# Kernel tuning notes

Measured on AMD Instinct MI355X. Metric: run time of the kernel, lower is better.

The kernel has to match this reference:

```python
import math
import jax, jax.numpy as jnp
import numpy as np

B, T, C, H = 2, 2048, 1024, 16
HD = C // H
ALPHA = 32.0


def setup_inputs() -> dict:
    key = jax.random.key(0)
    ks = jax.random.split(key, 16)
    s = 0.02
    inp = {
        "query": jax.random.normal(ks[0], (B, T, C), jnp.float32),
        "key": jax.random.normal(ks[1], (B, T, C), jnp.float32),
        "value": jax.random.normal(ks[2], (B, T, C), jnp.float32),
        # causal mask: 0 => masked (matches masked_fill(att_mask == 0, -inf))
        "att_mask": jnp.tril(jnp.ones((1, 1, T, T), jnp.float32)),
        "Wq": jax.random.normal(ks[3], (C, C), jnp.float32) * s,
        "bq": jnp.zeros((C,), jnp.float32),
        "Wk": jax.random.normal(ks[4], (C, C), jnp.float32) * s,
        "bk": jnp.zeros((C,), jnp.float32),
        "Wv": jax.random.normal(ks[5], (C, C), jnp.float32) * s,
        "bv": jnp.zeros((C,), jnp.float32),
        "Wp": jax.random.normal(ks[6], (C, C), jnp.float32) * s,
        "bp": jnp.zeros((C,), jnp.float32),
    }
    return inp


def reference(query, key, value, att_mask, Wq, bq, Wk, bk, Wv, bv, Wp, bp):
    b, tq, c = query.shape
    tk = key.shape[1]
    # separate QKV projections, split heads: [B,H,T,HD]
    q = (query @ Wq + bq).reshape(b, tq, H, HD).transpose(0, 2, 1, 3)
    k = (key @ Wk + bk).reshape(b, tk, H, HD).transpose(0, 2, 1, 3)
    v = (value @ Wv + bv).reshape(b, tk, H, HD).transpose(0, 2, 1, 3)
    # PBrelax: pre-scale q by 1/(alpha*sqrt(hd)), subtract detached global abs-max, rescale
    att = jnp.einsum("bhqd,bhkd->bhqk", q * (1.0 / ALPHA / math.sqrt(HD)), k)
    att = (att - jax.lax.stop_gradient(jnp.max(jnp.abs(att)))) * ALPHA
    att = jnp.where(att_mask[:, :, :tq, :tk] == 0, -jnp.inf, att)
    att = jax.nn.softmax(att, axis=-1)
    y = jnp.einsum("bhqk,bhkd->bhqd", att, v)
    y = y.transpose(0, 2, 1, 3).reshape(b, tq, c)
    return y @ Wp + bp
```

## Files before the change

kernel.cpp:

```cpp
#include <hip/hip_runtime.h>


#define Bsz 2
#define Tsz 2048
#define Csz 1024
#define Hsz 16
#define HDsz 64

typedef __bf16 bf16;
typedef __bf16 bf16x8 __attribute__((ext_vector_type(8)));
typedef __bf16 bf16x4 __attribute__((ext_vector_type(4)));
typedef float float4v __attribute__((ext_vector_type(4)));

#define MFMA16(a, b, c) __builtin_amdgcn_mfma_f32_16x16x32_bf16(a, b, c, 0, 0, 0)

#define GLOAD_LDS16(gptr, lptr)                                      \
  __builtin_amdgcn_global_load_lds(                                  \
      (const __attribute__((address_space(1))) void*)(gptr),         \
      (__attribute__((address_space(3))) void*)(lptr), 16, 0, 0)

__global__ __launch_bounds__(256) void cast3_bf16(
    const float* __restrict__ q, const float* __restrict__ k,
    const float* __restrict__ v, bf16* __restrict__ oq,
    bf16* __restrict__ ok, bf16* __restrict__ ov) {
  const int z = blockIdx.z;
  const float* src = z == 0 ? q : (z == 1 ? k : v);
  bf16* dst = z == 0 ? oq : (z == 1 ? ok : ov);
  const size_t i = ((size_t)blockIdx.x * 256 + threadIdx.x) * 8;
  const float4 a = *(const float4*)(src + i);
  const float4 b = *(const float4*)(src + i + 4);
  bf16x8 o;
  o[0] = (bf16)a.x; o[1] = (bf16)a.y; o[2] = (bf16)a.z; o[3] = (bf16)a.w;
  o[4] = (bf16)b.x; o[5] = (bf16)b.y; o[6] = (bf16)b.z; o[7] = (bf16)b.w;
  *(bf16x8*)(dst + i) = o;
}

__global__ __launch_bounds__(256) void wtrans_bf16(
    const float* __restrict__ Wq, const float* __restrict__ Wk,
    const float* __restrict__ Wv, const float* __restrict__ Wp,
    bf16* __restrict__ WT) {
  const int z = blockIdx.z;
  const float* W = z == 0 ? Wq : (z == 1 ? Wk : (z == 2 ? Wv : Wp));
  bf16* out = WT + (size_t)z * (Csz * Csz);
  __shared__ float Ts[64][68];
  const int k0 = blockIdx.y * 64, n0 = blockIdx.x * 64;
  const int tid = threadIdx.x;
#pragma unroll
  for (int it = 0; it < 4; ++it) {
    const int idx = it * 256 + tid;
    const int r = idx >> 4, c4 = (idx & 15) * 4;
    *(float4*)&Ts[r][c4] = *(const float4*)(W + (size_t)(k0 + r) * Csz + n0 + c4);
  }
  __syncthreads();
#pragma unroll
  for (int it = 0; it < 2; ++it) {
    const int idx = it * 256 + tid;
    const int n = idx & 63, k8 = (idx >> 6) * 8;
    bf16x8 o;
#pragma unroll
    for (int j = 0; j < 8; ++j) o[j] = (bf16)Ts[k8 + j][n];
    *(bf16x8*)(out + (size_t)(n0 + n) * Csz + k0 + k8) = o;
  }
}

__global__ __launch_bounds__(512, 2) void gemm256_qkv(
    const bf16* __restrict__ A0, const bf16* __restrict__ A1,
    const bf16* __restrict__ A2, const bf16* __restrict__ Wt,
    const float* __restrict__ b0, const float* __restrict__ b1,
    const float* __restrict__ b2, bf16* __restrict__ C0,
    bf16* __restrict__ C1, bf16* __restrict__ Vt) {
  constexpr int NT = Csz / 64;
  const int z = blockIdx.z;
  const bf16* A = z == 0 ? A0 : (z == 1 ? A1 : A2);
  const float* bias = z == 0 ? b0 : (z == 1 ? b1 : b2);
  const bf16* Bt = Wt + (size_t)z * (Csz * Csz);
  const int m0 = blockIdx.y * 256;
  const int nz0 = blockIdx.x * 256;

  __shared__ bf16 As[2 * 256 * 64];
  __shared__ bf16 Bs[2 * 256 * 64];

  const int tid = threadIdx.x;
  const int wave = tid >> 6, lane = tid & 63;
  const int l15 = lane & 15, quad = lane >> 4;
  const int wm = wave >> 2, wn = wave & 3;

  const int srow = tid >> 3;
  const int sch = tid & 7;
  const bf16* Ab = A + (size_t)(m0 + srow) * Csz + (sch ^ (srow & 7)) * 8;
  const bf16* Bb = Bt + (size_t)(nz0 + srow) * Csz + (sch ^ (srow & 7)) * 8;

#define STG(Xb, lds, lbuf, hh, tt)                                           \
  {                                                                          \
    GLOAD_LDS16((Xb) + (size_t)((hh)*128) * Csz + (size_t)(tt)*64,           \
                &(lds)[(lbuf) * (256 * 64) + (hh)*8192 + tid * 8]);          \
    GLOAD_LDS16((Xb) + (size_t)((hh)*128 + 64) * Csz + (size_t)(tt)*64,     \
                &(lds)[(lbuf) * (256 * 64) + (hh)*8192 + 4096 + tid * 8]);  \
  }
#define RD_A(dst, lbuf, i2, ks)                                              \
  dst = *(const bf16x8*)&As[(lbuf) * (256 * 64) +                            \
                            (wm * 128 + (i2)*16 + l15) * 64 +                \
                            ((((ks)*4 + quad) ^ (l15 & 7)) * 8)];
#define RD_B(dst, lbuf, j2, ks)                                              \
  dst = *(const bf16x8*)&Bs[(lbuf) * (256 * 64) +                            \
                            (wn * 64 + (j2)*16 + l15) * 64 +                 \
                            ((((ks)*4 + quad) ^ (l15 & 7)) * 8)];

  float4v acc[8][4];
#pragma unroll
  for (int i = 0; i < 8; ++i)
#pragma unroll
    for (int j = 0; j < 4; ++j) acc[i][j] = (float4v){0.f, 0.f, 0.f, 0.f};

  STG(Ab, As, 0, 0, 0);
  STG(Ab, As, 0, 1, 0);
  STG(Bb, Bs, 0, 0, 0);
  STG(Bb, Bs, 0, 1, 0);
  STG(Ab, As, 1, 0, 1);
  STG(Ab, As, 1, 1, 1);
  asm volatile("s_waitcnt vmcnt(4)" ::: "memory");
  __builtin_amdgcn_s_barrier();
  __builtin_amdgcn_sched_barrier(0);

#pragma unroll 1
  for (int t = 0; t < NT; ++t) {
    const int bsel = t & 1;
    bf16x8 af0[4][2], af1[4][2], bf0[2][2], bf1[2][2];

#pragma unroll
    for (int i = 0; i < 4; ++i) {
      RD_A(af0[i][0], bsel, i, 0);
      RD_A(af0[i][1], bsel, i, 1);
    }
#pragma unroll
    for (int j = 0; j < 2; ++j) {
      RD_B(bf0[j][0], bsel, j, 0);
      RD_B(bf0[j][1], bsel, j, 1);
    }
    if (t + 1 < NT) STG(Bb, Bs, bsel ^ 1, 0, t + 1);
    __builtin_amdgcn_s_barrier();
    asm volatile("s_waitcnt lgkmcnt(0)" ::: "memory");
    __builtin_amdgcn_sched_barrier(0);
    __builtin_amdgcn_s_setprio(1);
#pragma unroll
    for (int i = 0; i < 4; ++i)
#pragma unroll
      for (int j = 0; j < 2; ++j) {
        acc[i][j] = MFMA16(af0[i][0], bf0[j][0], acc[i][j]);
        acc[i][j] = MFMA16(af0[i][1], bf0[j][1], acc[i][j]);
      }
    __builtin_amdgcn_s_setprio(0);
    __builtin_amdgcn_s_barrier();

#pragma unroll
    for (int i = 0; i < 4; ++i) {
      RD_A(af1[i][0], bsel, 4 + i, 0);
      RD_A(af1[i][1], bsel, 4 + i, 1);
    }
    if (t + 1 < NT) STG(Bb, Bs, bsel ^ 1, 1, t + 1);
    __builtin_amdgcn_s_barrier();
    asm volatile("s_waitcnt lgkmcnt(0)" ::: "memory");
    __builtin_amdgcn_sched_barrier(0);
    __builtin_amdgcn_s_setprio(1);
#pragma unroll
    for (int i = 0; i < 4; ++i)
#pragma unroll
      for (int j = 0; j < 2; ++j) {
        acc[4 + i][j] = MFMA16(af1[i][0], bf0[j][0], acc[4 + i][j]);
        acc[4 + i][j] = MFMA16(af1[i][1], bf0[j][1], acc[4 + i][j]);
      }
    __builtin_amdgcn_s_setprio(0);
    __builtin_amdgcn_s_barrier();

#pragma unroll
    for (int j = 0; j < 2; ++j) {
      RD_B(bf1[j][0], bsel, 2 + j, 0);
      RD_B(bf1[j][1], bsel, 2 + j, 1);
    }
    if (t + 2 < NT) STG(Ab, As, bsel, 0, t + 2);
    __builtin_amdgcn_s_barrier();
    asm volatile("s_waitcnt lgkmcnt(0)" ::: "memory");
    __builtin_amdgcn_sched_barrier(0);
    __builtin_amdgcn_s_setprio(1);
#pragma unroll
    for (int i = 0; i < 4; ++i)
#pragma unroll
      for (int j = 0; j < 2; ++j) {
        acc[i][2 + j] = MFMA16(af0[i][0], bf1[j][0], acc[i][2 + j]);
        acc[i][2 + j] = MFMA16(af0[i][1], bf1[j][1], acc[i][2 + j]);
      }
    __builtin_amdgcn_s_setprio(0);
    __builtin_amdgcn_s_barrier();

    if (t + 2 < NT) STG(Ab, As, bsel, 1, t + 2);
    __builtin_amdgcn_s_barrier();
    __builtin_amdgcn_s_setprio(1);
#pragma unroll
    for (int i = 0; i < 4; ++i)
#pragma unroll
      for (int j = 0; j < 2; ++j) {
        acc[4 + i][2 + j] = MFMA16(af1[i][0], bf1[j][0], acc[4 + i][2 + j]);
        acc[4 + i][2 + j] = MFMA16(af1[i][1], bf1[j][1], acc[4 + i][2 + j]);
      }
    __builtin_amdgcn_s_setprio(0);
    if (t + 2 < NT) {
      asm volatile("s_waitcnt vmcnt(4)" ::: "memory");
    } else if (t + 1 < NT) {
      asm volatile("s_waitcnt vmcnt(0)" ::: "memory");
    }
    __builtin_amdgcn_s_barrier();
    __builtin_amdgcn_sched_barrier(0);
  }
#undef STG
#undef RD_A
#undef RD_B

  const int omb0 = m0 + wm * 128 + quad * 4;
  const int onb0 = nz0 + wn * 64 + l15;
  if (z == 2) {
#pragma unroll
    for (int j = 0; j < 4; ++j) {
      const int n = onb0 + j * 16;
      const float bj = bias[n];
#pragma unroll
      for (int i = 0; i < 8; ++i) {
        const int mrow = omb0 + i * 16;
        const int bb = mrow >> 11, tt = mrow & (Tsz - 1);
        union { bf16 h[4]; uint2 u; } pk;
#pragma unroll
        for (int r = 0; r < 4; ++r) pk.h[r] = (bf16)(acc[i][j][r] + bj);
        *(uint2*)(Vt + ((size_t)(bb * 1024 + n)) * Tsz + tt) = pk.u;
      }
    }
  } else {
    bf16* C = z == 0 ? C0 : C1;
    const float osc = z == 0 ? 0.180336880111124f : 1.0f;
#pragma unroll
    for (int j = 0; j < 4; ++j) {
      const float bj = bias[onb0 + j * 16];
#pragma unroll
      for (int i = 0; i < 8; ++i) {
#pragma unroll
        for (int r = 0; r < 4; ++r) {
          const float v = (acc[i][j][r] + bj) * osc;
          C[(size_t)(omb0 + i * 16 + r) * Csz + onb0 + j * 16] = (bf16)v;
        }
      }
    }
  }
}

template <typename OutT, bool VTR>
__global__ __launch_bounds__(256) void gemm_mfma(
    const bf16* __restrict__ A0, const bf16* __restrict__ A1,
    const bf16* __restrict__ A2, const bf16* __restrict__ Wt,
    const float* __restrict__ b0, const float* __restrict__ b1,
    const float* __restrict__ b2, OutT* __restrict__ C0,
    OutT* __restrict__ C1, OutT* __restrict__ C2, int M, int N, int K) {
  const int z = blockIdx.z;
  const bf16* A = z == 0 ? A0 : (z == 1 ? A1 : A2);
  const float* bias = z == 0 ? b0 : (z == 1 ? b1 : b2);
  OutT* C = z == 0 ? C0 : (z == 1 ? C1 : C2);
  const bf16* Bt = Wt + (size_t)z * N * K;
  const float osc = (VTR && z == 0) ? 0.180336880111124f : 1.0f;

  __shared__ bf16 As[128 * 32];
  __shared__ bf16 Bs[128 * 32];
  const int tid = threadIdx.x;
  const int wave = tid >> 6, lane = tid & 63;
  const int l15 = lane & 15, quad = lane >> 4;
  const int m0 = blockIdx.y * 128, n0 = blockIdx.x * 128;
  const int wm = (wave >> 1) * 64, wn = (wave & 1) * 64;
  const int srow = tid >> 2, schunk = tid & 3;

  float4v acc[4][4];
#pragma unroll
  for (int i = 0; i < 4; ++i)
#pragma unroll
    for (int j = 0; j < 4; ++j) acc[i][j] = (float4v){0.f, 0.f, 0.f, 0.f};

  for (int k0 = 0; k0 < K; k0 += 32) {
    __syncthreads();
#pragma unroll
    for (int p = 0; p < 2; ++p) {
      const int row = p * 64 + srow;
      GLOAD_LDS16(A + (size_t)(m0 + row) * K + k0 + schunk * 8,
                  &As[(p * 256 + tid) * 8]);
      GLOAD_LDS16(Bt + (size_t)(n0 + row) * K + k0 + schunk * 8,
                  &Bs[(p * 256 + tid) * 8]);
    }
    __syncthreads();

    bf16x8 af[4], bfr[4];
#pragma unroll
    for (int i = 0; i < 4; ++i)
      af[i] = *(const bf16x8*)&As[(wm + i * 16 + l15) * 32 + quad * 8];
#pragma unroll
    for (int j = 0; j < 4; ++j)
      bfr[j] = *(const bf16x8*)&Bs[(wn + j * 16 + l15) * 32 + quad * 8];
#pragma unroll
    for (int i = 0; i < 4; ++i)
#pragma unroll
      for (int j = 0; j < 4; ++j)
        acc[i][j] = MFMA16(af[i], bfr[j], acc[i][j]);
  }

  const int omb = m0 + wm + quad * 4;
  const int onb = n0 + wn + l15;
  if (VTR && z == 2) {
#pragma unroll
    for (int j = 0; j < 4; ++j) {
      const int n = onb + j * 16;
      const float bj = bias[n];
#pragma unroll
      for (int i = 0; i < 4; ++i) {
        const int mrow = omb + i * 16;
        const int bb = mrow >> 11, t = mrow & (Tsz - 1);
        union { bf16 h[4]; uint2 u; } pk;
#pragma unroll
        for (int r = 0; r < 4; ++r) pk.h[r] = (bf16)(acc[i][j][r] + bj);
        *(uint2*)((bf16*)C + ((size_t)(bb * 1024 + n)) * Tsz + t) = pk.u;
      }
    }
  } else {
#pragma unroll
    for (int j = 0; j < 4; ++j) {
      const float bj = bias[onb + j * 16];
#pragma unroll
      for (int i = 0; i < 4; ++i) {
#pragma unroll
        for (int r = 0; r < 4; ++r) {
          const float v = (acc[i][j][r] + bj) * osc;
          const size_t off = (size_t)(omb + i * 16 + r) * N + onb + j * 16;
          if constexpr (sizeof(OutT) == 2)
            C[off] = (OutT)v;
          else
            C[off] = v;
        }
      }
    }
  }
}

__global__ __launch_bounds__(256) void attn_mfma(const bf16* __restrict__ Q,
                                                 const bf16* __restrict__ K,
                                                 const bf16* __restrict__ Vt,
                                                 bf16* __restrict__ Y) {
  __shared__ bf16 Ks[2][64 * 64];
  __shared__ bf16 Vs[2][64 * 64];
  __shared__ bf16 Ps[4][32 * 72];

  const int bh = blockIdx.y;
  const int b = bh >> 4, h = bh & 15;
  const int i0 = (int)(gridDim.x - 1 - blockIdx.x) * 128;
  const int tid = threadIdx.x;
  const int wave = tid >> 6, lane = tid & 63;
  const int l15 = lane & 15, quad = lane >> 4;

  const int srow = tid >> 3;
  const int sch = tid & 7;

  const bf16* kb = K + (size_t)b * Tsz * Csz + h * HDsz;
  const bf16* vb = Vt + (size_t)bh * HDsz * Tsz;

  const int qb = i0 + wave * 32;

  bf16x8 qf[2][2];
#pragma unroll
  for (int sub = 0; sub < 2; ++sub) {
    const bf16* qp =
        Q + ((size_t)(b * Tsz + qb + sub * 16 + l15)) * Csz + h * HDsz + quad * 8;
    qf[sub][0] = *(const bf16x8*)qp;
    qf[sub][1] = *(const bf16x8*)(qp + 32);
  }

  bf16x8 ones;
#pragma unroll
  for (int j = 0; j < 8; ++j) ones[j] = (bf16)1.0f;

  float4v Of[2][4];
  float4v accl[2];
#pragma unroll
  for (int sub = 0; sub < 2; ++sub) {
    accl[sub] = (float4v){0.f, 0.f, 0.f, 0.f};
#pragma unroll
    for (int nc = 0; nc < 4; ++nc) Of[sub][nc] = (float4v){0.f, 0.f, 0.f, 0.f};
  }

  const int ntile = i0 / 64 + 2;

#pragma unroll
  for (int p = 0; p < 2; ++p) {
    const int r = p * 32 + srow;
    const int c = sch ^ (r & 7);
    GLOAD_LDS16(kb + (size_t)r * Csz + c * 8, &Ks[0][(p * 256 + tid) * 8]);
    GLOAD_LDS16(vb + (size_t)r * Tsz + c * 8, &Vs[0][(p * 256 + tid) * 8]);
  }

  for (int t = 0; t < ntile; ++t) {
    const int j0 = t * 64;
    const int buf = t & 1;
    __syncthreads();
    if (t + 1 < ntile) {
#pragma unroll
      for (int p = 0; p < 2; ++p) {
        const int r = p * 32 + srow;
        const int c = sch ^ (r & 7);
        GLOAD_LDS16(kb + (size_t)(j0 + 64 + r) * Csz + c * 8,
                    &Ks[buf ^ 1][(p * 256 + tid) * 8]);
        GLOAD_LDS16(vb + (size_t)r * Tsz + (j0 + 64) + c * 8,
                    &Vs[buf ^ 1][(p * 256 + tid) * 8]);
      }
    }

    if (j0 <= qb + 31) {
      float4v S[2][4];
#pragma unroll
      for (int nc = 0; nc < 4; ++nc) {
        const int row = nc * 16 + l15;
        const bf16x8 k0 =
            *(const bf16x8*)&Ks[buf][row * 64 + ((quad ^ (row & 7)) * 8)];
        const bf16x8 k1 =
            *(const bf16x8*)&Ks[buf][row * 64 + (((quad + 4) ^ (row & 7)) * 8)];
#pragma unroll
        for (int sub = 0; sub < 2; ++sub) {
          float4v a = (float4v){0.f, 0.f, 0.f, 0.f};
          a = MFMA16(k0, qf[sub][0], a);
          a = MFMA16(k1, qf[sub][1], a);
          S[sub][nc] = a;
        }
      }

      if (j0 + 63 > qb) {
#pragma unroll
        for (int sub = 0; sub < 2; ++sub) {
          const int q = qb + sub * 16 + l15;
#pragma unroll
          for (int nc = 0; nc < 4; ++nc) {
            const int keyb = j0 + nc * 16 + quad * 4;
#pragma unroll
            for (int r = 0; r < 4; ++r)
              if (keyb + r > q) S[sub][nc][r] = -1e30f;
          }
        }
      }

#pragma unroll
      for (int sub = 0; sub < 2; ++sub) {
#pragma unroll
        for (int nc = 0; nc < 4; ++nc) {
          bf16x4 pk;
#pragma unroll
          for (int r = 0; r < 4; ++r)
            pk[r] = (bf16)__builtin_amdgcn_exp2f(S[sub][nc][r]);
          *(bf16x4*)&Ps[wave][(sub * 16 + l15) * 72 + nc * 16 + quad * 4] = pk;
        }
      }

      bf16x8 pf[2][2];
#pragma unroll
      for (int sub = 0; sub < 2; ++sub) {
#pragma unroll
        for (int kc = 0; kc < 2; ++kc)
          pf[sub][kc] = *(const bf16x8*)
              &Ps[wave][(sub * 16 + l15) * 72 + kc * 32 + quad * 8];
        accl[sub] = MFMA16(ones, pf[sub][0], accl[sub]);
        accl[sub] = MFMA16(ones, pf[sub][1], accl[sub]);
      }
#pragma unroll
      for (int nc = 0; nc < 4; ++nc) {
        const int row = nc * 16 + l15;
#pragma unroll
        for (int kc = 0; kc < 2; ++kc) {
          const bf16x8 vf = *(const bf16x8*)
              &Vs[buf][row * 64 + (((kc * 4 + quad) ^ (row & 7)) * 8)];
#pragma unroll
          for (int sub = 0; sub < 2; ++sub)
            Of[sub][nc] = MFMA16(vf, pf[sub][kc], Of[sub][nc]);
        }
      }
    }
  }

#pragma unroll
  for (int sub = 0; sub < 2; ++sub) {
    const float rl = __builtin_amdgcn_rcpf(accl[sub][0]);
    const size_t rowoff =
        ((size_t)(b * Tsz + qb + sub * 16 + l15)) * Csz + h * HDsz;
#pragma unroll
    for (int nc = 0; nc < 4; ++nc) {
      union { bf16 h4[4]; uint2 u; } pk;
#pragma unroll
      for (int r = 0; r < 4; ++r) pk.h4[r] = (bf16)(Of[sub][nc][r] * rl);
      *(uint2*)(Y + rowoff + nc * 16 + quad * 4) = pk.u;
    }
  }
}

extern "C" void kernel_launch(void* const* d_in, const int* in_sizes, int n_in,
                              void* d_out, int out_size, void* d_ws,
                              size_t ws_size, hipStream_t stream) {
  const float* query = (const float*)d_in[0];
  const float* key = (const float*)d_in[1];
  const float* value = (const float*)d_in[2];
  const float* Wq = (const float*)d_in[4];
  const float* bq = (const float*)d_in[5];
  const float* Wk = (const float*)d_in[6];
  const float* bk = (const float*)d_in[7];
  const float* Wv = (const float*)d_in[8];
  const float* bv = (const float*)d_in[9];
  const float* Wp = (const float*)d_in[10];
  const float* bp = (const float*)d_in[11];
  float* out = (float*)d_out;

  char* ws = (char*)d_ws;
  bf16* WT = (bf16*)(ws);
  bf16* vc = (bf16*)(ws + (8u << 20));
  bf16* Qp = (bf16*)(ws + (16u << 20));
  bf16* Kp = (bf16*)(ws + (24u << 20));
  bf16* Vt = (bf16*)(ws + (32u << 20));
  bf16* Yb = vc;
  bf16* qc = (bf16*)d_out;
  bf16* kc = (bf16*)((char*)d_out + (8u << 20));

  const int M = Bsz * Tsz;

  cast3_bf16<<<dim3((M * Csz) / (256 * 8), 1, 3), dim3(256), 0, stream>>>(
      query, key, value, qc, kc, vc);
  wtrans_bf16<<<dim3(16, 16, 4), dim3(256), 0, stream>>>(Wq, Wk, Wv, Wp, WT);
  gemm256_qkv<<<dim3(Csz / 256, M / 256, 3), dim3(512), 0, stream>>>(
      qc, kc, vc, WT, bq, bk, bv, Qp, Kp, Vt);
  attn_mfma<<<dim3(Tsz / 128, Bsz * Hsz), dim3(256), 0, stream>>>(Qp, Kp, Vt,
                                                                  Yb);
  gemm_mfma<float, false><<<dim3(Csz / 128, M / 128, 1), dim3(256), 0, stream>>>(
      Yb, Yb, Yb, WT + 3u * (Csz * Csz), bp, bp, bp, out, out, out, M, Csz,
      Csz);
}
```

Baseline: 257.0 us.

## Triple-buffer K/V tiles with explicit vmcnt waits and balance causal block order

Moves the attention kernel's K/V staging from double to triple buffering and prefetches two tiles ahead. Partial vmcnt waits plus raw s_barrier replace __syncthreads, so the next tile's loads can stay in flight while the current tile is computed. It also interleaves query-block indices (long and short causal rows alternate, mirrored for the second batch) to balance work across CUs. The cost is higher LDS use per block, which may lower occupancy, and hand-written waitcnt logic that depends on the exact count of outstanding loads.

```diff
diff --git a/kernel.cpp b/kernel.cpp
--- a/kernel.cpp
+++ b/kernel.cpp
@@ -346,13 +346,16 @@
                                                  const bf16* __restrict__ K,
                                                  const bf16* __restrict__ Vt,
                                                  bf16* __restrict__ Y) {
-  __shared__ bf16 Ks[2][64 * 64];
-  __shared__ bf16 Vs[2][64 * 64];
+  __shared__ bf16 Ks[3][64 * 64];
+  __shared__ bf16 Vs[3][64 * 64];
   __shared__ bf16 Ps[4][32 * 72];
 
   const int bh = blockIdx.y;
   const int b = bh >> 4, h = bh & 15;
-  const int i0 = (int)(gridDim.x - 1 - blockIdx.x) * 128;
+  int xr = (blockIdx.x & 1) ? (int)(gridDim.x - 1 - (blockIdx.x >> 1))
+                            : (int)(blockIdx.x >> 1);
+  if (bh >= 16) xr = (int)(gridDim.x - 1) - xr;
+  const int i0 = xr * 128;
   const int tid = threadIdx.x;
   const int wave = tid >> 6, lane = tid & 63;
   const int l15 = lane & 15, quad = lane >> 4;
@@ -389,29 +392,30 @@
 
   const int ntile = i0 / 64 + 2;
 
-#pragma unroll
-  for (int p = 0; p < 2; ++p) {
-    const int r = p * 32 + srow;
-    const int c = sch ^ (r & 7);
-    GLOAD_LDS16(kb + (size_t)r * Csz + c * 8, &Ks[0][(p * 256 + tid) * 8]);
-    GLOAD_LDS16(vb + (size_t)r * Tsz + c * 8, &Vs[0][(p * 256 + tid) * 8]);
-  }
-
+#define STAGE_KV(tt, bb)                                                     \
+  {                                                                          \
+    _Pragma("unroll") for (int p = 0; p < 2; ++p) {                          \
+      const int r = p * 32 + srow;                                           \
+      const int c = sch ^ (r & 7);                                           \
+      GLOAD_LDS16(kb + (size_t)((tt)*64 + r) * Csz + c * 8,                  \
+                  &Ks[bb][(p * 256 + tid) * 8]);                             \
+      GLOAD_LDS16(vb + (size_t)r * Tsz + (tt)*64 + c * 8,                    \
+                  &Vs[bb][(p * 256 + tid) * 8]);                             \
+    }                                                                        \
+  }
+
+  STAGE_KV(0, 0);
+  STAGE_KV(1, 1);
+  asm volatile("s_waitcnt vmcnt(4)" ::: "memory");
+  __builtin_amdgcn_s_barrier();
+  __builtin_amdgcn_sched_barrier(0);
+
+  int bcur = 0;
+#pragma unroll 1
   for (int t = 0; t < ntile; ++t) {
     const int j0 = t * 64;
-    const int buf = t & 1;
-    __syncthreads();
-    if (t + 1 < ntile) {
-#pragma unroll
-      for (int p = 0; p < 2; ++p) {
-        const int r = p * 32 + srow;
-        const int c = sch ^ (r & 7);
-        GLOAD_LDS16(kb + (size_t)(j0 + 64 + r) * Csz + c * 8,
-                    &Ks[buf ^ 1][(p * 256 + tid) * 8]);
-        GLOAD_LDS16(vb + (size_t)r * Tsz + (j0 + 64) + c * 8,
-                    &Vs[buf ^ 1][(p * 256 + tid) * 8]);
-      }
-    }
+    const int bst = bcur == 0 ? 2 : bcur - 1;
+    if (t + 2 < ntile) STAGE_KV(t + 2, bst);
 
     if (j0 <= qb + 31) {
       float4v S[2][4];
@@ -419,9 +423,9 @@
       for (int nc = 0; nc < 4; ++nc) {
         const int row = nc * 16 + l15;
         const bf16x8 k0 =
-            *(const bf16x8*)&Ks[buf][row * 64 + ((quad ^ (row & 7)) * 8)];
+            *(const bf16x8*)&Ks[bcur][row * 64 + ((quad ^ (row & 7)) * 8)];
         const bf16x8 k1 =
-            *(const bf16x8*)&Ks[buf][row * 64 + (((quad + 4) ^ (row & 7)) * 8)];
+            *(const bf16x8*)&Ks[bcur][row * 64 + (((quad + 4) ^ (row & 7)) * 8)];
 #pragma unroll
         for (int sub = 0; sub < 2; ++sub) {
           float4v a = (float4v){0.f, 0.f, 0.f, 0.f};
@@ -473,14 +477,25 @@
 #pragma unroll
         for (int kc = 0; kc < 2; ++kc) {
           const bf16x8 vf = *(const bf16x8*)
-              &Vs[buf][row * 64 + (((kc * 4 + quad) ^ (row & 7)) * 8)];
+              &Vs[bcur][row * 64 + (((kc * 4 + quad) ^ (row & 7)) * 8)];
 #pragma unroll
           for (int sub = 0; sub < 2; ++sub)
             Of[sub][nc] = MFMA16(vf, pf[sub][kc], Of[sub][nc]);
         }
       }
     }
-  }
+
+    if (t + 2 < ntile) {
+      asm volatile("s_waitcnt vmcnt(4)" ::: "memory");
+    } else if (t + 1 < ntile) {
+      asm volatile("s_waitcnt vmcnt(0)" ::: "memory");
+    }
+    __builtin_amdgcn_sched_barrier(0);
+    __builtin_amdgcn_s_barrier();
+    __builtin_amdgcn_sched_barrier(0);
+    bcur = bcur == 2 ? 0 : bcur + 1;
+  }
+#undef STAGE_KV
 
 #pragma unroll
   for (int sub = 0; sub < 2; ++sub) {
```

Result: faster. 248.7 us (-3.2%).
